# Performance work log

Hardware: AMD Instinct MI355X
Metric: run time of the kernel (lower is better)

The kernel has to match this reference:

```python
import jax, jax.numpy as jnp
import numpy as np

N, E, F, T = 10000, 160000, 4, 12   # nodes, edges, features, periods
C, HID, OUT = 512, 256, 12          # tgcn out_channels, head hidden, output_dim


def setup_inputs() -> dict:
    key = jax.random.key(0)
    ks = jax.random.split(key, 24)
    g = lambda k, s: (jax.random.normal(k, s, dtype=jnp.float32) * 0.05)
    inp = {
        "x": jax.random.normal(ks[0], (N, F, T), dtype=jnp.float32),
        "edge_index": jax.random.randint(ks[1], (2, E), 0, N, dtype=jnp.int32),
        "edge_attr": jax.random.uniform(ks[2], (E,), dtype=jnp.float32),
        "att": g(ks[3], (T,)),
        # TGCN gates: GCNConv (W [F,C], b [C]) + Linear on cat([conv, H]) ([2C,C], [C])
        "Wz_g": g(ks[4], (F, C)), "bz_g": jnp.zeros((C,), jnp.float32),
        "Wz_l": g(ks[5], (2 * C, C)), "bz_l": jnp.zeros((C,), jnp.float32),
        "Wr_g": g(ks[6], (F, C)), "br_g": jnp.zeros((C,), jnp.float32),
        "Wr_l": g(ks[7], (2 * C, C)), "br_l": jnp.zeros((C,), jnp.float32),
        "Wh_g": g(ks[8], (F, C)), "bh_g": jnp.zeros((C,), jnp.float32),
        "Wh_l": g(ks[9], (2 * C, C)), "bh_l": jnp.zeros((C,), jnp.float32),
        # dense head
        "W1": g(ks[10], (C, HID)), "b1": jnp.zeros((HID,), jnp.float32),
        "W2": g(ks[11], (HID, OUT)), "b2": jnp.zeros((OUT,), jnp.float32),
    }
    return inp


def reference(x, edge_index, edge_attr, att,
              Wz_g, bz_g, Wz_l, bz_l,
              Wr_g, br_g, Wr_l, br_l,
              Wh_g, bh_g, Wh_l, bh_l,
              W1, b1, W2, b2):
    n = x.shape[0]
    # GCN normalization with self loops (fill value 1.0), computed once
    loops = jnp.arange(n, dtype=edge_index.dtype)
    src = jnp.concatenate([edge_index[0], loops])
    dst = jnp.concatenate([edge_index[1], loops])
    w = jnp.concatenate([edge_attr, jnp.ones((n,), x.dtype)])
    deg = jax.ops.segment_sum(w, dst, num_segments=n)
    dinv = jax.lax.rsqrt(jnp.maximum(deg, 1e-12))
    norm = dinv[src] * w * dinv[dst]  # [E+N]

    def gcn(xt, W, b):
        xw = xt @ W                                   # [N,C]
        msg = norm[:, None] * xw[src]                 # gather over edges
        return jax.ops.segment_sum(msg, dst, num_segments=n) + b

    probs = jax.nn.softmax(att)            # attention over periods
    xt_seq = jnp.moveaxis(x, -1, 0)        # [T,N,F]
    H0 = jnp.zeros((n, C), x.dtype)

    def step(carry, inp):
        H, acc = carry
        xt, p = inp
        z = jax.nn.sigmoid(jnp.concatenate([gcn(xt, Wz_g, bz_g), H], axis=1) @ Wz_l + bz_l)
        r = jax.nn.sigmoid(jnp.concatenate([gcn(xt, Wr_g, br_g), H], axis=1) @ Wr_l + br_l)
        ht = jnp.tanh(jnp.concatenate([gcn(xt, Wh_g, bh_g), H * r], axis=1) @ Wh_l + bh_l)
        Hn = z * H + (1.0 - z) * ht
        return (Hn, acc + p * Hn), None

    (Hf, H_accum), _ = jax.lax.scan(step, (H0, H0), (xt_seq, probs))
    out_hidden = H_accum
    h = jax.nn.relu(H_accum)
    h = jax.nn.relu(h @ W1 + b1)
    h = h @ W2 + b2
    return (h, out_hidden)
```

## Files before the change

### kernel.cpp

```cpp
#include <hip/hip_runtime.h>
#include <math.h>

#define NF 48
#define TT 12

typedef __bf16 v8bf __attribute__((ext_vector_type(8)));
typedef float v16f __attribute__((ext_vector_type(16)));

__device__ __forceinline__ void gld16(const void* g, void* l) {
  __builtin_amdgcn_global_load_lds(
      (const __attribute__((address_space(1))) void*)(uintptr_t)g,
      (__attribute__((address_space(3))) void*)(uintptr_t)l, 16, 0, 0);
}


__global__ void k_init(float* __restrict__ deg, int* __restrict__ cnt, int n) {
  int i = blockIdx.x * blockDim.x + threadIdx.x;
  if (i < n) { deg[i] = 1.0f; cnt[i] = 0; cnt[n + i] = 0; }
}

__global__ void k_edge(const int* __restrict__ dst, const float* __restrict__ w,
                       float* __restrict__ deg, int* __restrict__ cnt, int e) {
  int i = blockIdx.x * blockDim.x + threadIdx.x;
  if (i < e) {
    int d = dst[i];
    atomicAdd(&deg[d], w[i]);
    atomicAdd(&cnt[d], 1);
  }
}


__global__ void k_scan1(const int* __restrict__ cnt, int* __restrict__ pscan,
                        int* __restrict__ bsum, const float* __restrict__ deg,
                        float* __restrict__ dinv, int n) {
  __shared__ int s[256];
  int i = blockIdx.x * 256 + threadIdx.x;
  int v = (i < n) ? cnt[i] : 0;
  s[threadIdx.x] = v;
  __syncthreads();
  for (int off = 1; off < 256; off <<= 1) {
    int t = 0;
    if (threadIdx.x >= off) t = s[threadIdx.x - off];
    __syncthreads();
    s[threadIdx.x] += t;
    __syncthreads();
  }
  if (i < n) {
    pscan[i] = s[threadIdx.x] - v;
    dinv[i] = rsqrtf(fmaxf(deg[i], 1e-12f));
  }
  if (threadIdx.x == 255) bsum[blockIdx.x] = s[255];
}

__global__ void k_scan2(const int* __restrict__ bsum, int* __restrict__ bpre, int nb,
                        const float* __restrict__ att, float* __restrict__ probs) {
  if (blockIdx.x == 0 && threadIdx.x == 0) {
    int run = 0;
    for (int b = 0; b < nb; b++) { bpre[b] = run; run += bsum[b]; }
  }
  if (blockIdx.x == 0 && threadIdx.x == 64) {
    float m = -1e30f;
    for (int t = 0; t < TT; t++) m = fmaxf(m, att[t]);
    float e[TT], s = 0.f;
    for (int t = 0; t < TT; t++) { e[t] = expf(att[t] - m); s += e[t]; }
    for (int t = 0; t < TT; t++) probs[t] = e[t] / s;
  }
}

__global__ void k_scan3(const int* __restrict__ pscan, const int* __restrict__ bpre,
                        int* __restrict__ offs, int n, int e) {
  int i = blockIdx.x * blockDim.x + threadIdx.x;
  if (i < n) offs[i] = pscan[i] + bpre[i >> 8];
  if (i == 0) offs[n] = e;
}

__global__ void k_place(const int* __restrict__ src, const int* __restrict__ dst,
                        const float* __restrict__ w, const int* __restrict__ offs,
                        int* __restrict__ fill, int* __restrict__ csrc,
                        float* __restrict__ cw, int e) {
  int i = blockIdx.x * blockDim.x + threadIdx.x;
  if (i >= e) return;
  int d = dst[i];
  int p = offs[d] + atomicAdd(&fill[d], 1);
  csrc[p] = src[i];
  cw[p] = w[i];
}

__global__ void k_gather(const int* __restrict__ offs, const int* __restrict__ csrc,
                         const float* __restrict__ cw, const float* __restrict__ dinv,
                         const float* __restrict__ x, float* __restrict__ Y, int n) {
  int tg = blockIdx.x * blockDim.x + threadIdx.x;
  if (tg >= n * 12) return;
  int i = tg / 12, q = tg % 12;
  float di = dinv[i];
  const float4* x4 = (const float4*)x;
  float4 sv = x4[(size_t)i * 12 + q];
  float ax = di * sv.x, ay = di * sv.y, az = di * sv.z, aw = di * sv.w;
  int e1 = offs[i + 1];
  for (int e = offs[i]; e < e1; e++) {
    int s = csrc[e];
    float wv = cw[e] * dinv[s];
    float4 xv = x4[(size_t)s * 12 + q];
    ax = fmaf(wv, xv.x, ax); ay = fmaf(wv, xv.y, ay);
    az = fmaf(wv, xv.z, az); aw = fmaf(wv, xv.w, aw);
  }
  float4 o = make_float4(di * ax, di * ay, di * az, di * aw);
  ((float4*)Y)[(size_t)i * 12 + q] = o;
}

__device__ __forceinline__ size_t packIdx128(int n, int k) {
  int row = n & 127;
  int c = (k & 31) >> 3;
  return (size_t)(n >> 7) * (128 * 512) + (size_t)(k >> 5) * (128 * 32) +
         (size_t)row * 32 + (size_t)((c ^ ((row >> 1) & 3)) << 3) + (k & 7);
}

__global__ void k_pack3(const float* __restrict__ Wzl, const float* __restrict__ Wrl,
                        const float* __restrict__ Whl, const float* __restrict__ W1,
                        __bf16* __restrict__ WzrP, __bf16* __restrict__ WhP,
                        __bf16* __restrict__ W1P) {
  __shared__ __bf16 t[64][72];
  int modew = blockIdx.z;
  if (modew == 1 && blockIdx.x >= 8) return;
  if (modew == 2 && blockIdx.x >= 4) return;
  int n0 = blockIdx.x * 64, k0 = blockIdx.y * 64;
  __bf16* WT = (modew == 0) ? WzrP : (modew == 1) ? WhP : W1P;
#pragma unroll
  for (int p = 0; p < 4; p++) {
    int kk = p * 16 + (threadIdx.x >> 4);
    int nn = (threadIdx.x & 15) * 4;
    int n = n0 + nn, k = k0 + kk;
    float4 v;
    if (modew == 2) {
      v = *(const float4*)(W1 + (size_t)k * 256 + n);
    } else {
      const float* src = (modew == 1) ? Whl : Wzl;
      int nc = n;
      if (modew == 0 && n >= 512) { src = Wrl; nc = n - 512; }
      v = *(const float4*)(src + (size_t)(512 + k) * 512 + nc);
    }
    t[kk][nn + 0] = (__bf16)v.x; t[kk][nn + 1] = (__bf16)v.y;
    t[kk][nn + 2] = (__bf16)v.z; t[kk][nn + 3] = (__bf16)v.w;
  }
  __syncthreads();
#pragma unroll
  for (int u = 0; u < 2; u++) {
    int unit = threadIdx.x * 2 + u;
    int nl = unit >> 3, kg = unit & 7;
    v8bf o;
#pragma unroll
    for (int j = 0; j < 8; j++) o[j] = t[kg * 8 + j][nl];
    *(v8bf*)(WT + packIdx128(n0 + nl, k0 + kg * 8)) = o;
  }
}

__global__ void k_build_eff3(const float* __restrict__ Wzg, const float* __restrict__ Wzl,
                             const float* __restrict__ bzg, const float* __restrict__ bzl,
                             const float* __restrict__ Wrg, const float* __restrict__ Wrl,
                             const float* __restrict__ brg, const float* __restrict__ brl,
                             const float* __restrict__ Whg, const float* __restrict__ Whl,
                             const float* __restrict__ bhg, const float* __restrict__ bhl,
                             float* __restrict__ WzrE, float* __restrict__ bzrE,
                             float* __restrict__ WhE, float* __restrict__ bhE) {
  int idx = blockIdx.x * blockDim.x + threadIdx.x;
  if (idx >= 3 * 5 * 512) return;
  int seg = idx / 2560;
  int r = (idx % 2560) / 512, c = idx % 512;
  const float *Wg, *Wl, *bg, *bl;
  float *We, *be;
  int ostride, ooff;
  if (seg == 0) { Wg = Wzg; Wl = Wzl; bg = bzg; bl = bzl; We = WzrE; be = bzrE; ostride = 1024; ooff = 0; }
  else if (seg == 1) { Wg = Wrg; Wl = Wrl; bg = brg; bl = brl; We = WzrE; be = bzrE; ostride = 1024; ooff = 512; }
  else { Wg = Whg; Wl = Whl; bg = bhg; bl = bhl; We = WhE; be = bhE; ostride = 512; ooff = 0; }
  float s = 0.f;
  if (r < 4) {
    for (int k = 0; k < 512; k++) s += Wg[r * 512 + k] * Wl[k * 512 + c];
    We[r * ostride + ooff + c] = s;
  } else {
    for (int k = 0; k < 512; k++) s += bg[k] * Wl[k * 512 + c];
    be[ooff + c] = s + bl[c];
  }
}

__global__ void k_wy3(const float* __restrict__ WzrE, const float* __restrict__ bzrE,
                      const float* __restrict__ WhE, const float* __restrict__ bhE,
                      const float* __restrict__ b1,
                      __bf16* __restrict__ WyZR, __bf16* __restrict__ WyH,
                      __bf16* __restrict__ Wy1) {
  int idx = blockIdx.x * blockDim.x + threadIdx.x;
  const float* Weff; const float* beff; __bf16* out; int Nout, loc;
  if (idx < 1024 * 16) { Weff = WzrE; beff = bzrE; out = WyZR; Nout = 1024; loc = idx; }
  else if (idx < (1024 + 512) * 16) { Weff = WhE; beff = bhE; out = WyH; Nout = 512; loc = idx - 1024 * 16; }
  else if (idx < (1024 + 512 + 256) * 16) { Weff = nullptr; beff = b1; out = Wy1; Nout = 256; loc = idx - (1024 + 512) * 16; }
  else return;
  int n = loc >> 4, k = loc & 15;
  float v = 0.f;
  if (k < 4) v = Weff ? Weff[k * Nout + n] : 0.f;
  else if (k == 4) v = beff[n];
  out[(size_t)(n >> 7) * 2048 + (size_t)(n & 127) * 16 + k] = (__bf16)v;
}

__global__ void k_yat0(const float* __restrict__ Y,
                       const float* __restrict__ WzrE, const float* __restrict__ bzrE,
                       const float* __restrict__ WhE, const float* __restrict__ bhE,
                       __bf16* __restrict__ Ya, __bf16* __restrict__ H1, int n) {
  int idx = blockIdx.x * blockDim.x + threadIdx.x;
  int nt0 = n * 512;
  if (idx < nt0) {
    int i = idx >> 9, c = idx & 511;
    float y0 = Y[(size_t)i * NF + 0], y1 = Y[(size_t)i * NF + 12];
    float y2 = Y[(size_t)i * NF + 24], y3 = Y[(size_t)i * NF + 36];
    float pz = bzrE[c] + y0 * WzrE[c] + y1 * WzrE[1024 + c] +
               y2 * WzrE[2048 + c] + y3 * WzrE[3072 + c];
    float ph = bhE[c] + y0 * WhE[c] + y1 * WhE[512 + c] +
               y2 * WhE[1024 + c] + y3 * WhE[1536 + c];
    float z = 1.f / (1.f + expf(-pz));
    H1[idx] = (__bf16)((1.f - z) * tanhf(ph));
  } else {
    int r = idx - nt0;
    if (r >= TT * n * 16) return;
    int t = r / (n * 16);
    int loc = r % (n * 16);
    int nn = loc >> 4, k = loc & 15;
    float v = 0.f;
    if (k < 4) v = Y[(size_t)nn * NF + k * TT + t];
    else if (k == 4) v = 1.f;
    Ya[r] = (__bf16)v;
  }
}

template <int MODE>
__global__ __launch_bounds__(256, 4) void k_mm(
    const __bf16* __restrict__ Agm, const __bf16* __restrict__ Bp,
    const __bf16* __restrict__ Hc, const __bf16* __restrict__ Zbf,
    const __bf16* __restrict__ Ay, const __bf16* __restrict__ Wy,
    float* __restrict__ Ofp, __bf16* __restrict__ Obf, __bf16* __restrict__ ObfR,
    int M, int RB) {
  constexpr int BUFS = 6144;
  __shared__ __bf16 smem[21504];

  const int RBX = (RB + 7) >> 3;
  {
    int xcd = blockIdx.x & 7;
    int idx = blockIdx.x >> 3;
    int rowblk = xcd * RBX + idx % RBX;
    int colblk = idx / RBX;
    if (rowblk >= RB) return;

    const int row0 = rowblk * 64;
    const int tid = threadIdx.x;
    const int lane = tid & 63, w = tid >> 6;
    const int wr = (w >> 1) * 32, wc = (w & 1) * 64;
    const int l31 = lane & 31, lh = lane >> 5;

    const int ar = tid >> 2, ac = tid & 3;
    const __bf16* At = Agm + (size_t)(row0 + ar) * 512 + ((ac ^ ((ar >> 1) & 3)) << 3);
    const __bf16* Bt = Bp + (size_t)colblk * (128 * 512);

    v16f acc[2];
#pragma unroll
    for (int j = 0; j < 2; j++)
#pragma unroll
      for (int q = 0; q < 16; q++) acc[j][q] = 0.f;

    auto stage = [&](int buf, int kt) {
      __bf16* base = smem + buf * BUFS;
      gld16(At + kt * 32, base + w * 512);
      const __bf16* bs = Bt + (size_t)kt * 4096 + (size_t)tid * 8;
      gld16(bs, base + 2048 + w * 512);
      gld16(bs + 2048, base + 4096 + w * 512);
    };
    auto stageY = [&]() {
      if (w < 2)
        gld16(Ay + (size_t)(row0 + (tid >> 1)) * 16 + (tid & 1) * 8,
              smem + 18432 + w * 512);
      gld16(Wy + (size_t)colblk * 2048 + (size_t)tid * 8, smem + 19456 + w * 512);
    };
    auto compute = [&](int buf) {
      const __bf16* base = smem + buf * BUFS;
      __builtin_amdgcn_s_setprio(1);
#pragma unroll
      for (int ks = 0; ks < 2; ks++) {
        int kc = ks * 2 + lh;
        int fr = wr + l31;
        v8bf a = *(const v8bf*)&base[fr * 32 + ((kc ^ ((fr >> 1) & 3)) << 3)];
#pragma unroll
        for (int ni = 0; ni < 2; ni++) {
          int fc = wc + ni * 32 + l31;
          v8bf b = *(const v8bf*)&base[2048 + fc * 32 + ((kc ^ ((fc >> 1) & 3)) << 3)];
          acc[ni] = __builtin_amdgcn_mfma_f32_32x32x16_bf16(a, b, acc[ni], 0, 0, 0);
        }
      }
      __builtin_amdgcn_s_setprio(0);
    };
    auto computeY = [&]() {
      const __bf16* ya = smem + 18432;
      const __bf16* yb = smem + 19456;
      v8bf a = *(const v8bf*)&ya[(wr + l31) * 16 + lh * 8];
#pragma unroll
      for (int ni = 0; ni < 2; ni++) {
        v8bf b = *(const v8bf*)&yb[(wc + ni * 32 + l31) * 16 + lh * 8];
        acc[ni] = __builtin_amdgcn_mfma_f32_32x32x16_bf16(a, b, acc[ni], 0, 0, 0);
      }
    };

    stageY();
    stage(0, 0);
    stage(1, 1);
#pragma unroll
    for (int kt = 0; kt < 16; kt++) {
      if (kt < 15)
        asm volatile("s_waitcnt vmcnt(3) lgkmcnt(0)\n\ts_barrier" ::: "memory");
      else
        asm volatile("s_waitcnt vmcnt(0) lgkmcnt(0)\n\ts_barrier" ::: "memory");
      if (kt < 14) stage((kt + 2) % 3, kt + 2);
      compute(kt % 3);
    }
    computeY();
    __syncthreads();

    if constexpr (MODE == 2) {
#pragma unroll
      for (int ni = 0; ni < 2; ni++) {
        int cl = wc + ni * 32 + l31;
#pragma unroll
        for (int reg = 0; reg < 16; reg++) {
          int rg = row0 + wr + (reg & 3) + ((reg >> 2) << 3) + (lh << 2);
          if (rg >= M) continue;
          Ofp[(size_t)rg * 256 + colblk * 128 + cl] = fmaxf(acc[ni][reg], 0.f);
        }
      }
    } else if constexpr (MODE == 0) {
#pragma unroll
      for (int ni = 0; ni < 2; ni++) {
        int cl = wc + ni * 32 + l31;
#pragma unroll
        for (int reg = 0; reg < 16; reg++) {
          int lr = wr + (reg & 3) + ((reg >> 2) << 3) + (lh << 2);
          smem[lr * 128 + cl] = (__bf16)(1.f / (1.f + expf(-acc[ni][reg])));
        }
      }
      __syncthreads();
      int row = tid >> 2, seg = (tid & 3) * 32;
      int rg = row0 + row;
      if (rg < M) {
        int cof = (colblk & 3) * 128;
        if (colblk < 4) {
#pragma unroll
          for (int q = 0; q < 4; q++) {
            uint4 v = *(const uint4*)&smem[row * 128 + seg + q * 8];
            *(uint4*)(Obf + (size_t)rg * 512 + cof + seg + q * 8) = v;
          }
        } else {
#pragma unroll
          for (int q = 0; q < 4; q++) {
            v8bf r8 = *(const v8bf*)&smem[row * 128 + seg + q * 8];
            v8bf h8 = *(const v8bf*)(Agm + (size_t)rg * 512 + cof + seg + q * 8);
            v8bf o;
#pragma unroll
            for (int j = 0; j < 8; j++) o[j] = (__bf16)((float)r8[j] * (float)h8[j]);
            *(v8bf*)(ObfR + (size_t)rg * 512 + cof + seg + q * 8) = o;
          }
        }
      }
    } else {
      float* sF = (float*)smem;
#pragma unroll
      for (int h = 0; h < 2; h++) {
        if ((w >> 1) == h) {
#pragma unroll
          for (int ni = 0; ni < 2; ni++) {
            int cl = wc + ni * 32 + l31;
#pragma unroll
            for (int reg = 0; reg < 16; reg++) {
              int lr = (reg & 3) + ((reg >> 2) << 3) + (lh << 2);
              sF[lr * 128 + cl] = tanhf(acc[ni][reg]);
            }
          }
        }
        __syncthreads();
        int row = tid >> 3, seg = (tid & 7) * 16;
        int rg = row0 + h * 32 + row;
        if (rg < M) {
          int cg0 = colblk * 128 + seg;
#pragma unroll
          for (int q = 0; q < 2; q++) {
            v8bf z8 = *(const v8bf*)(Zbf + (size_t)rg * 512 + cg0 + q * 8);
            v8bf h8 = *(const v8bf*)(Hc + (size_t)rg * 512 + cg0 + q * 8);
            v8bf o;
#pragma unroll
            for (int j = 0; j < 8; j++) {
              float z = (float)z8[j];
              float ht = sF[row * 128 + seg + q * 8 + j];
              o[j] = (__bf16)(z * (float)h8[j] + (1.f - z) * ht);
            }
            *(v8bf*)(Obf + (size_t)rg * 512 + cg0 + q * 8) = o;
          }
        }
        if (h == 0) __syncthreads();
      }
    }
  }
}

__global__ void k_acc(const __bf16* __restrict__ hist, const float* __restrict__ probs,
                      float* __restrict__ acc, __bf16* __restrict__ accRelu, int n) {
  int idx = blockIdx.x * blockDim.x + threadIdx.x;
  if (idx >= n * 64) return;
  size_t off = (size_t)idx * 8;
  size_t S = (size_t)n * 512;
  float s[8] = {0, 0, 0, 0, 0, 0, 0, 0};
#pragma unroll
  for (int t = 0; t < TT; t++) {
    float p = probs[t];
    v8bf h = *(const v8bf*)(hist + (size_t)(t + 1) * S + off);
#pragma unroll
    for (int j = 0; j < 8; j++) s[j] = fmaf(p, (float)h[j], s[j]);
  }
  *(float4*)(acc + off) = make_float4(s[0], s[1], s[2], s[3]);
  *(float4*)(acc + off + 4) = make_float4(s[4], s[5], s[6], s[7]);
  v8bf rl;
#pragma unroll
  for (int j = 0; j < 8; j++) rl[j] = (__bf16)fmaxf(s[j], 0.f);
  *(v8bf*)(accRelu + off) = rl;
}

__global__ void k_head2(const float* __restrict__ T1, const float* __restrict__ W2,
                        const float* __restrict__ b2, float* __restrict__ out0, int M) {
  int idx = blockIdx.x * blockDim.x + threadIdx.x;
  if (idx >= M * 12) return;
  int i = idx / 12, c = idx % 12;
  const float* tr = T1 + (size_t)i * 256;
  float s = b2[c];
  for (int k = 0; k < 256; k++) s = fmaf(tr[k], W2[k * 12 + c], s);
  out0[idx] = s;
}


extern "C" void kernel_launch(void* const* d_in, const int* in_sizes, int n_in,
                              void* d_out, int out_size, void* d_ws, size_t ws_size,
                              hipStream_t stream) {
  const float* x   = (const float*)d_in[0];
  const int*   ei  = (const int*)d_in[1];
  const float* ea  = (const float*)d_in[2];
  const float* att = (const float*)d_in[3];
  const float* Wzg = (const float*)d_in[4];  const float* bzg = (const float*)d_in[5];
  const float* Wzl = (const float*)d_in[6];  const float* bzl = (const float*)d_in[7];
  const float* Wrg = (const float*)d_in[8];  const float* brg = (const float*)d_in[9];
  const float* Wrl = (const float*)d_in[10]; const float* brl = (const float*)d_in[11];
  const float* Whg = (const float*)d_in[12]; const float* bhg = (const float*)d_in[13];
  const float* Whl = (const float*)d_in[14]; const float* bhl = (const float*)d_in[15];
  const float* W1  = (const float*)d_in[16]; const float* b1  = (const float*)d_in[17];
  const float* W2  = (const float*)d_in[18]; const float* b2  = (const float*)d_in[19];

  const int N = in_sizes[0] / NF;
  const int E = in_sizes[1] / 2;
  const int* srcI = ei;
  const int* dstI = ei + E;

  float* out0 = (float*)d_out;
  float* accO = (float*)d_out + (size_t)N * 12;

  char* wp = (char*)d_ws;
  auto carve = [&](size_t bytes) -> void* {
    void* p = (void*)wp;
    wp += (bytes + 255) & ~(size_t)255;
    return p;
  };
  float*  deg     = (float*)carve((size_t)N * 4);
  float*  dinv    = (float*)carve((size_t)N * 4);
  float*  probs   = (float*)carve(64);
  float*  Y       = (float*)carve((size_t)N * NF * 4);
  __bf16* WzrP    = (__bf16*)carve((size_t)1024 * 512 * 2);
  __bf16* WhP     = (__bf16*)carve((size_t)512 * 512 * 2);
  __bf16* W1P     = (__bf16*)carve((size_t)256 * 512 * 2);
  float*  Wzr_eff = (float*)carve((size_t)4 * 1024 * 4);
  float*  bzr_eff = (float*)carve((size_t)1024 * 4);
  float*  Wh_eff  = (float*)carve((size_t)4 * 512 * 4);
  float*  bh_eff  = (float*)carve((size_t)512 * 4);
  __bf16* hist    = (__bf16*)carve((size_t)(TT + 1) * N * 512 * 2);
  __bf16* Zbf     = (__bf16*)carve((size_t)N * 512 * 2);
  __bf16* Rbf     = (__bf16*)carve((size_t)N * 512 * 2);
  __bf16* accRelu = (__bf16*)carve((size_t)N * 512 * 2);
  float*  T1      = (float*)carve((size_t)N * 256 * 4);
  __bf16* Ya      = (__bf16*)carve((size_t)TT * N * 16 * 2);
  __bf16* WyZR    = (__bf16*)carve((size_t)1024 * 16 * 2);
  __bf16* WyH    = (__bf16*)carve((size_t)512 * 16 * 2);
  __bf16* Wy1     = (__bf16*)carve((size_t)256 * 16 * 2);
  int*    cnt     = (int*)carve((size_t)2 * N * 4);
  int*    fill    = cnt + N;
  int*    offs    = (int*)carve((size_t)(N + 1) * 4);
  int*    pscan   = (int*)carve((size_t)N * 4);
  int*    bsum    = (int*)carve(256);
  int*    bpre    = (int*)carve(256);
  int*    csrc    = (int*)carve((size_t)E * 4);
  float*  cw      = (float*)carve((size_t)E * 4);
  (void)carve(512 * 1024);
  (void)ws_size; (void)n_in; (void)out_size;

  const int TPB = 256;
  auto cdiv = [](int a, int b) { return (a + b - 1) / b; };
  const size_t S = (size_t)N * 512;

  k_init<<<cdiv(N, TPB), TPB, 0, stream>>>(deg, cnt, N);
  k_edge<<<cdiv(E, TPB), TPB, 0, stream>>>(dstI, ea, deg, cnt, E);

  const int nb = cdiv(N, 256);
  k_scan1<<<nb, 256, 0, stream>>>(cnt, pscan, bsum, deg, dinv, N);
  k_scan2<<<1, 128, 0, stream>>>(bsum, bpre, nb, att, probs);
  k_scan3<<<cdiv(N, TPB), TPB, 0, stream>>>(pscan, bpre, offs, N, E);
  k_place<<<cdiv(E, TPB), TPB, 0, stream>>>(srcI, dstI, ea, offs, fill, csrc, cw, E);
  k_gather<<<cdiv(N * 12, TPB), TPB, 0, stream>>>(offs, csrc, cw, dinv, x, Y, N);

  {
    dim3 gp(16, 8, 3);
    k_pack3<<<gp, 256, 0, stream>>>(Wzl, Wrl, Whl, W1, WzrP, WhP, W1P);
  }
  k_build_eff3<<<cdiv(3 * 5 * 512, TPB), TPB, 0, stream>>>(
      Wzg, Wzl, bzg, bzl, Wrg, Wrl, brg, brl, Whg, Whl, bhg, bhl,
      Wzr_eff, bzr_eff, Wh_eff, bh_eff);
  k_wy3<<<cdiv((1024 + 512 + 256) * 16, TPB), TPB, 0, stream>>>(
      Wzr_eff, bzr_eff, Wh_eff, bh_eff, b1, WyZR, WyH, Wy1);

  k_yat0<<<cdiv(N * 512 + TT * N * 16, TPB), TPB, 0, stream>>>(
      Y, Wzr_eff, bzr_eff, Wh_eff, bh_eff, Ya, hist + S, N);

  const int RB = cdiv(N, 64);
  const int RBX = cdiv(RB, 8);
  for (int t = 1; t < TT; t++) {
    const __bf16* Hbt = hist + (size_t)t * S;
    __bf16* Hbn = hist + (size_t)(t + 1) * S;
    const __bf16* Yat = Ya + (size_t)t * N * 16;
    k_mm<0><<<8 * RBX * 8, 256, 0, stream>>>(Hbt, WzrP, nullptr, nullptr, Yat, WyZR,
                                             nullptr, Zbf, Rbf, N, RB);
    k_mm<1><<<8 * RBX * 4, 256, 0, stream>>>(Rbf, WhP, Hbt, Zbf, Yat, WyH,
                                             nullptr, Hbn, nullptr, N, RB);
  }

  k_acc<<<cdiv(N * 64, TPB), TPB, 0, stream>>>(hist, probs, accO, accRelu, N);
  k_mm<2><<<8 * RBX * 2, 256, 0, stream>>>(accRelu, W1P, nullptr, nullptr, Ya, Wy1,
                                           T1, nullptr, nullptr, N, RB);
  k_head2<<<cdiv(N * 12, TPB), TPB, 0, stream>>>(T1, W2, b2, out0, N);
}
```

Before: 673.0 us.

## Enlarge GEMM block tile to 128x128 with 512-thread blocks

The recurrent GEMM kernel now processes 128 rows per block with 8 waves instead of 64 rows with 4 waves. Each B-tile stage in LDS is shared by twice as many rows, which halves global B traffic per output and the number of blocks. Staging, wait counts and the MODE 1 epilogue (now four 32-row passes) are adjusted to match. The risks are register pressure under launch_bounds(512,4) and lower occupancy from the larger LDS footprint.

```diff
diff --git a/kernel.cpp b/kernel.cpp
--- a/kernel.cpp
+++ b/kernel.cpp
@@ -230,175 +230,167 @@
 }
 
 template <int MODE>
-__global__ __launch_bounds__(256, 4) void k_mm(
+__global__ __launch_bounds__(512, 4) void k_mm(
     const __bf16* __restrict__ Agm, const __bf16* __restrict__ Bp,
     const __bf16* __restrict__ Hc, const __bf16* __restrict__ Zbf,
     const __bf16* __restrict__ Ay, const __bf16* __restrict__ Wy,
     float* __restrict__ Ofp, __bf16* __restrict__ Obf, __bf16* __restrict__ ObfR,
     int M, int RB) {
-  constexpr int BUFS = 6144;
-  __shared__ __bf16 smem[21504];
+  constexpr int BUFS = 8192;
+  __shared__ __bf16 smem[28672];
+  constexpr int AYOFF = 24576, WYOFF = 26624;
 
   const int RBX = (RB + 7) >> 3;
-  {
-    int xcd = blockIdx.x & 7;
-    int idx = blockIdx.x >> 3;
-    int rowblk = xcd * RBX + idx % RBX;
-    int colblk = idx / RBX;
-    if (rowblk >= RB) return;
-
-    const int row0 = rowblk * 64;
-    const int tid = threadIdx.x;
-    const int lane = tid & 63, w = tid >> 6;
-    const int wr = (w >> 1) * 32, wc = (w & 1) * 64;
-    const int l31 = lane & 31, lh = lane >> 5;
-
-    const int ar = tid >> 2, ac = tid & 3;
-    const __bf16* At = Agm + (size_t)(row0 + ar) * 512 + ((ac ^ ((ar >> 1) & 3)) << 3);
-    const __bf16* Bt = Bp + (size_t)colblk * (128 * 512);
-
-    v16f acc[2];
-#pragma unroll
-    for (int j = 0; j < 2; j++)
-#pragma unroll
-      for (int q = 0; q < 16; q++) acc[j][q] = 0.f;
-
-    auto stage = [&](int buf, int kt) {
-      __bf16* base = smem + buf * BUFS;
-      gld16(At + kt * 32, base + w * 512);
-      const __bf16* bs = Bt + (size_t)kt * 4096 + (size_t)tid * 8;
-      gld16(bs, base + 2048 + w * 512);
-      gld16(bs + 2048, base + 4096 + w * 512);
-    };
-    auto stageY = [&]() {
-      if (w < 2)
-        gld16(Ay + (size_t)(row0 + (tid >> 1)) * 16 + (tid & 1) * 8,
-              smem + 18432 + w * 512);
-      gld16(Wy + (size_t)colblk * 2048 + (size_t)tid * 8, smem + 19456 + w * 512);
-    };
-    auto compute = [&](int buf) {
-      const __bf16* base = smem + buf * BUFS;
-      __builtin_amdgcn_s_setprio(1);
-#pragma unroll
-      for (int ks = 0; ks < 2; ks++) {
-        int kc = ks * 2 + lh;
-        int fr = wr + l31;
-        v8bf a = *(const v8bf*)&base[fr * 32 + ((kc ^ ((fr >> 1) & 3)) << 3)];
-#pragma unroll
-        for (int ni = 0; ni < 2; ni++) {
-          int fc = wc + ni * 32 + l31;
-          v8bf b = *(const v8bf*)&base[2048 + fc * 32 + ((kc ^ ((fc >> 1) & 3)) << 3)];
-          acc[ni] = __builtin_amdgcn_mfma_f32_32x32x16_bf16(a, b, acc[ni], 0, 0, 0);
+  int xcd = blockIdx.x & 7;
+  int idx = blockIdx.x >> 3;
+  int rowblk = xcd * RBX + idx % RBX;
+  int colblk = idx / RBX;
+  if (rowblk >= RB) return;
+
+  const int row0 = rowblk * 128;
+  const int tid = threadIdx.x;
+  const int lane = tid & 63, w = tid >> 6;
+  const int wr = (w >> 1) * 32, wc = (w & 1) * 64;
+  const int l31 = lane & 31, lh = lane >> 5;
+
+  const int ar = tid >> 2, ac = tid & 3;
+  const __bf16* At = Agm + (size_t)(row0 + ar) * 512 + ((ac ^ ((ar >> 1) & 3)) << 3);
+  const __bf16* Bt = Bp + (size_t)colblk * (128 * 512);
+
+  v16f acc[2];
+#pragma unroll
+  for (int j = 0; j < 2; j++)
+#pragma unroll
+    for (int q = 0; q < 16; q++) acc[j][q] = 0.f;
+
+  auto stage = [&](int buf, int kt) {
+    __bf16* base = smem + buf * BUFS;
+    gld16(At + kt * 32, base + w * 512);
+    gld16(Bt + (size_t)kt * 4096 + (size_t)tid * 8, base + 4096 + w * 512);
+  };
+  auto stageY = [&]() {
+    if (tid < 256) {
+      gld16(Ay + (size_t)(row0 + (tid >> 1)) * 16 + (tid & 1) * 8, smem + AYOFF + w * 512);
+      gld16(Wy + (size_t)colblk * 2048 + (size_t)tid * 8, smem + WYOFF + w * 512);
+    }
+  };
+  auto compute = [&](int buf) {
+    const __bf16* base = smem + buf * BUFS;
+    __builtin_amdgcn_s_setprio(1);
+#pragma unroll
+    for (int ks = 0; ks < 2; ks++) {
+      int kc = ks * 2 + lh;
+      int fr = wr + l31;
+      v8bf a = *(const v8bf*)&base[fr * 32 + ((kc ^ ((fr >> 1) & 3)) << 3)];
+#pragma unroll
+      for (int ni = 0; ni < 2; ni++) {
+        int fc = wc + ni * 32 + l31;
+        v8bf b = *(const v8bf*)&base[4096 + fc * 32 + ((kc ^ ((fc >> 1) & 3)) << 3)];
+        acc[ni] = __builtin_amdgcn_mfma_f32_32x32x16_bf16(a, b, acc[ni], 0, 0, 0);
+      }
+    }
+    __builtin_amdgcn_s_setprio(0);
+  };
+  auto computeY = [&]() {
+    v8bf a = *(const v8bf*)&smem[AYOFF + (wr + l31) * 16 + lh * 8];
+#pragma unroll
+    for (int ni = 0; ni < 2; ni++) {
+      v8bf b = *(const v8bf*)&smem[WYOFF + (wc + ni * 32 + l31) * 16 + lh * 8];
+      acc[ni] = __builtin_amdgcn_mfma_f32_32x32x16_bf16(a, b, acc[ni], 0, 0, 0);
+    }
+  };
+
+  stageY();
+  stage(0, 0);
+  stage(1, 1);
+#pragma unroll
+  for (int kt = 0; kt < 16; kt++) {
+    if (kt < 15)
+      asm volatile("s_waitcnt vmcnt(2) lgkmcnt(0)\n\ts_barrier" ::: "memory");
+    else
+      asm volatile("s_waitcnt vmcnt(0) lgkmcnt(0)\n\ts_barrier" ::: "memory");
+    if (kt < 14) stage((kt + 2) % 3, kt + 2);
+    compute(kt % 3);
+  }
+  computeY();
+  __syncthreads();
+
+  if constexpr (MODE == 2) {
+#pragma unroll
+    for (int ni = 0; ni < 2; ni++) {
+      int cl = wc + ni * 32 + l31;
+#pragma unroll
+      for (int reg = 0; reg < 16; reg++) {
+        int rg = row0 + wr + (reg & 3) + ((reg >> 2) << 3) + (lh << 2);
+        if (rg >= M) continue;
+        Ofp[(size_t)rg * 256 + colblk * 128 + cl] = fmaxf(acc[ni][reg], 0.f);
+      }
+    }
+  } else if constexpr (MODE == 0) {
+#pragma unroll
+    for (int ni = 0; ni < 2; ni++) {
+      int cl = wc + ni * 32 + l31;
+#pragma unroll
+      for (int reg = 0; reg < 16; reg++) {
+        int lr = wr + (reg & 3) + ((reg >> 2) << 3) + (lh << 2);
+        smem[lr * 128 + cl] = (__bf16)(1.f / (1.f + expf(-acc[ni][reg])));
+      }
+    }
+    __syncthreads();
+    int row = tid >> 2, seg = (tid & 3) * 32;
+    int rg = row0 + row;
+    if (rg < M) {
+      int cof = (colblk & 3) * 128;
+      if (colblk < 4) {
+#pragma unroll
+        for (int q = 0; q < 4; q++) {
+          uint4 v = *(const uint4*)&smem[row * 128 + seg + q * 8];
+          *(uint4*)(Obf + (size_t)rg * 512 + cof + seg + q * 8) = v;
+        }
+      } else {
+#pragma unroll
+        for (int q = 0; q < 4; q++) {
+          v8bf r8 = *(const v8bf*)&smem[row * 128 + seg + q * 8];
+          v8bf h8 = *(const v8bf*)(Agm + (size_t)rg * 512 + cof + seg + q * 8);
+          v8bf o;
+#pragma unroll
+          for (int j = 0; j < 8; j++) o[j] = (__bf16)((float)r8[j] * (float)h8[j]);
+          *(v8bf*)(ObfR + (size_t)rg * 512 + cof + seg + q * 8) = o;
         }
       }
-      __builtin_amdgcn_s_setprio(0);
-    };
-    auto computeY = [&]() {
-      const __bf16* ya = smem + 18432;
-      const __bf16* yb = smem + 19456;
-      v8bf a = *(const v8bf*)&ya[(wr + l31) * 16 + lh * 8];
-#pragma unroll
-      for (int ni = 0; ni < 2; ni++) {
-        v8bf b = *(const v8bf*)&yb[(wc + ni * 32 + l31) * 16 + lh * 8];
-        acc[ni] = __builtin_amdgcn_mfma_f32_32x32x16_bf16(a, b, acc[ni], 0, 0, 0);
-      }
-    };
-
-    stageY();
-    stage(0, 0);
-    stage(1, 1);
-#pragma unroll
-    for (int kt = 0; kt < 16; kt++) {
-      if (kt < 15)
-        asm volatile("s_waitcnt vmcnt(3) lgkmcnt(0)\n\ts_barrier" ::: "memory");
-      else
-        asm volatile("s_waitcnt vmcnt(0) lgkmcnt(0)\n\ts_barrier" ::: "memory");
-      if (kt < 14) stage((kt + 2) % 3, kt + 2);
-      compute(kt % 3);
-    }
-    computeY();
-    __syncthreads();
-
-    if constexpr (MODE == 2) {
-#pragma unroll
-      for (int ni = 0; ni < 2; ni++) {
-        int cl = wc + ni * 32 + l31;
-#pragma unroll
-        for (int reg = 0; reg < 16; reg++) {
-          int rg = row0 + wr + (reg & 3) + ((reg >> 2) << 3) + (lh << 2);
-          if (rg >= M) continue;
-          Ofp[(size_t)rg * 256 + colblk * 128 + cl] = fmaxf(acc[ni][reg], 0.f);
-        }
-      }
-    } else if constexpr (MODE == 0) {
-#pragma unroll
-      for (int ni = 0; ni < 2; ni++) {
-        int cl = wc + ni * 32 + l31;
-#pragma unroll
-        for (int reg = 0; reg < 16; reg++) {
-          int lr = wr + (reg & 3) + ((reg >> 2) << 3) + (lh << 2);
-          smem[lr * 128 + cl] = (__bf16)(1.f / (1.f + expf(-acc[ni][reg])));
+    }
+  } else {
+    float* sF = (float*)smem;
+#pragma unroll
+    for (int h = 0; h < 4; h++) {
+      if ((w >> 1) == h) {
+#pragma unroll
+        for (int ni = 0; ni < 2; ni++) {
+          int cl = wc + ni * 32 + l31;
+#pragma unroll
+          for (int reg = 0; reg < 16; reg++) {
+            int lr = (reg & 3) + ((reg >> 2) << 3) + (lh << 2);
+            sF[lr * 128 + cl] = tanhf(acc[ni][reg]);
+          }
         }
       }
       __syncthreads();
-      int row = tid >> 2, seg = (tid & 3) * 32;
-      int rg = row0 + row;
+      int row = tid >> 4, seg = (tid & 15) * 8;
+      int rg = row0 + h * 32 + row;
       if (rg < M) {
-        int cof = (colblk & 3) * 128;
-        if (colblk < 4) {
-#pragma unroll
-          for (int q = 0; q < 4; q++) {
-            uint4 v = *(const uint4*)&smem[row * 128 + seg + q * 8];
-            *(uint4*)(Obf + (size_t)rg * 512 + cof + seg + q * 8) = v;
-          }
-        } else {
-#pragma unroll
-          for (int q = 0; q < 4; q++) {
-            v8bf r8 = *(const v8bf*)&smem[row * 128 + seg + q * 8];
-            v8bf h8 = *(const v8bf*)(Agm + (size_t)rg * 512 + cof + seg + q * 8);
-            v8bf o;
-#pragma unroll
-            for (int j = 0; j < 8; j++) o[j] = (__bf16)((float)r8[j] * (float)h8[j]);
-            *(v8bf*)(ObfR + (size_t)rg * 512 + cof + seg + q * 8) = o;
-          }
+        int cg0 = colblk * 128 + seg;
+        v8bf z8 = *(const v8bf*)(Zbf + (size_t)rg * 512 + cg0);
+        v8bf h8 = *(const v8bf*)(Hc + (size_t)rg * 512 + cg0);
+        v8bf o;
+#pragma unroll
+        for (int j = 0; j < 8; j++) {
+          float z = (float)z8[j];
+          float ht = sF[row * 128 + seg + j];
+          o[j] = (__bf16)(z * (float)h8[j] + (1.f - z) * ht);
         }
+        *(v8bf*)(Obf + (size_t)rg * 512 + cg0) = o;
       }
-    } else {
-      float* sF = (float*)smem;
-#pragma unroll
-      for (int h = 0; h < 2; h++) {
-        if ((w >> 1) == h) {
-#pragma unroll
-          for (int ni = 0; ni < 2; ni++) {
-            int cl = wc + ni * 32 + l31;
-#pragma unroll
-            for (int reg = 0; reg < 16; reg++) {
-              int lr = (reg & 3) + ((reg >> 2) << 3) + (lh << 2);
-              sF[lr * 128 + cl] = tanhf(acc[ni][reg]);
-            }
-          }
-        }
-        __syncthreads();
-        int row = tid >> 3, seg = (tid & 7) * 16;
-        int rg = row0 + h * 32 + row;
-        if (rg < M) {
-          int cg0 = colblk * 128 + seg;
-#pragma unroll
-          for (int q = 0; q < 2; q++) {
-            v8bf z8 = *(const v8bf*)(Zbf + (size_t)rg * 512 + cg0 + q * 8);
-            v8bf h8 = *(const v8bf*)(Hc + (size_t)rg * 512 + cg0 + q * 8);
-            v8bf o;
-#pragma unroll
-            for (int j = 0; j < 8; j++) {
-              float z = (float)z8[j];
-              float ht = sF[row * 128 + seg + q * 8 + j];
-              o[j] = (__bf16)(z * (float)h8[j] + (1.f - z) * ht);
-            }
-            *(v8bf*)(Obf + (size_t)rg * 512 + cg0 + q * 8) = o;
-          }
-        }
-        if (h == 0) __syncthreads();
-      }
+      if (h < 3) __syncthreads();
     }
   }
 }
@@ -485,7 +477,7 @@
   float*  T1      = (float*)carve((size_t)N * 256 * 4);
   __bf16* Ya      = (__bf16*)carve((size_t)TT * N * 16 * 2);
   __bf16* WyZR    = (__bf16*)carve((size_t)1024 * 16 * 2);
-  __bf16* WyH    = (__bf16*)carve((size_t)512 * 16 * 2);
+  __bf16* WyH     = (__bf16*)carve((size_t)512 * 16 * 2);
   __bf16* Wy1     = (__bf16*)carve((size_t)256 * 16 * 2);
   int*    cnt     = (int*)carve((size_t)2 * N * 4);
   int*    fill    = cnt + N;
@@ -525,20 +517,20 @@
   k_yat0<<<cdiv(N * 512 + TT * N * 16, TPB), TPB, 0, stream>>>(
       Y, Wzr_eff, bzr_eff, Wh_eff, bh_eff, Ya, hist + S, N);
 
-  const int RB = cdiv(N, 64);
+  const int RB = cdiv(N, 128);
   const int RBX = cdiv(RB, 8);
   for (int t = 1; t < TT; t++) {
     const __bf16* Hbt = hist + (size_t)t * S;
     __bf16* Hbn = hist + (size_t)(t + 1) * S;
     const __bf16* Yat = Ya + (size_t)t * N * 16;
-    k_mm<0><<<8 * RBX * 8, 256, 0, stream>>>(Hbt, WzrP, nullptr, nullptr, Yat, WyZR,
+    k_mm<0><<<8 * RBX * 8, 512, 0, stream>>>(Hbt, WzrP, nullptr, nullptr, Yat, WyZR,
                                              nullptr, Zbf, Rbf, N, RB);
-    k_mm<1><<<8 * RBX * 4, 256, 0, stream>>>(Rbf, WhP, Hbt, Zbf, Yat, WyH,
+    k_mm<1><<<8 * RBX * 4, 512, 0, stream>>>(Rbf, WhP, Hbt, Zbf, Yat, WyH,
                                              nullptr, Hbn, nullptr, N, RB);
   }
 
   k_acc<<<cdiv(N * 64, TPB), TPB, 0, stream>>>(hist, probs, accO, accRelu, N);
-  k_mm<2><<<8 * RBX * 2, 256, 0, stream>>>(accRelu, W1P, nullptr, nullptr, Ya, Wy1,
+  k_mm<2><<<8 * RBX * 2, 512, 0, stream>>>(accRelu, W1P, nullptr, nullptr, Ya, Wy1,
                                            T1, nullptr, nullptr, N, RB);
   k_head2<<<cdiv(N * 12, TPB), TPB, 0, stream>>>(T1, W2, b2, out0, N);
 }
```

New measurement: 765.7 us. 13.8% more time.
